# Performance work log

Measured on AMD Instinct MI355X. Metric: run time of the kernel, lower is better.

Reference implementation:

```python
import jax, jax.numpy as jnp
import numpy as np

NUM_HEADS = 4

def setup_inputs() -> dict:
    key = jax.random.key(0)
    ks = jax.random.split(key, 9)
    total_nodes, d, hidden, B = 262144, 256, 256, 8192
    node_embeddings = jax.random.normal(ks[0], (total_nodes, d), dtype=jnp.float32)
    segment_ids = jnp.sort(jax.random.randint(ks[1], (total_nodes,), 0, B, dtype=jnp.int32))
    # learnable params (MultiheadAttention packed qkv, out_proj, query, output_proj)
    s = 0.05
    query = jax.random.normal(ks[2], (1, d), dtype=jnp.float32)
    in_proj_w = jax.random.normal(ks[3], (3 * d, d), dtype=jnp.float32) * s
    in_proj_b = jax.random.normal(ks[4], (3 * d,), dtype=jnp.float32) * s
    out_proj_w = jax.random.normal(ks[5], (d, d), dtype=jnp.float32) * s
    out_proj_b = jax.random.normal(ks[6], (d,), dtype=jnp.float32) * s
    output_proj_w = jax.random.normal(ks[7], (hidden, d), dtype=jnp.float32) * s
    output_proj_b = jax.random.normal(ks[8], (hidden,), dtype=jnp.float32) * s
    return {
        "node_embeddings": node_embeddings,
        "query": query,
        "in_proj_w": in_proj_w,
        "in_proj_b": in_proj_b,
        "out_proj_w": out_proj_w,
        "out_proj_b": out_proj_b,
        "output_proj_w": output_proj_w,
        "output_proj_b": output_proj_b,
        "segment_ids": segment_ids,
        "batch_size": B,
    }


def reference(node_embeddings, query, in_proj_w, in_proj_b, out_proj_w, out_proj_b,
              output_proj_w, output_proj_b, segment_ids, batch_size):
    # Ragged single-query cross-attention pooling (eval mode: dropout off).
    N, d = node_embeddings.shape
    H = NUM_HEADS
    dh = d // H
    Wq, Wk, Wv = in_proj_w[:d], in_proj_w[d:2 * d], in_proj_w[2 * d:]
    bq, bk, bv = in_proj_b[:d], in_proj_b[d:2 * d], in_proj_b[2 * d:]
    # query is shared across all graphs; torch MHA scales q by 1/sqrt(dh)
    q = ((query @ Wq.T + bq) / jnp.sqrt(jnp.asarray(dh, node_embeddings.dtype))).reshape(H, dh)
    k = (node_embeddings @ Wk.T + bk).reshape(N, H, dh)
    v = (node_embeddings @ Wv.T + bv).reshape(N, H, dh)
    scores = jnp.einsum('nhd,hd->nh', k, q)  # [N, H]
    # segment-wise stable softmax over ragged node groups
    m = jax.ops.segment_max(scores, segment_ids, num_segments=batch_size)  # [B, H]
    m = jnp.where(jnp.isfinite(m), m, 0.0)
    e = jnp.exp(scores - m[segment_ids])  # [N, H]
    denom = jax.ops.segment_sum(e, segment_ids, num_segments=batch_size)  # [B, H]
    numer = jax.ops.segment_sum(e[:, :, None] * v, segment_ids, num_segments=batch_size)  # [B, H, dh]
    attn = jnp.where(denom[:, :, None] > 0, numer / jnp.maximum(denom[:, :, None], 1e-30), 0.0)
    pooled = attn.reshape(batch_size, d) @ out_proj_w.T + out_proj_b  # MHA out_proj
    out = pooled @ output_proj_w.T + output_proj_b  # [B, hidden]
    # empty graphs -> zeros (matches torch branch), not just bias
    counts = jax.ops.segment_sum(jnp.ones((N,), out.dtype), segment_ids, num_segments=batch_size)
    return jnp.where(counts[:, None] > 0, out, 0.0)
```

## Files before the change

kernel.cpp:

```cpp
#include <hip/hip_runtime.h>
#include <hip/hip_bf16.h>
#include <stdint.h>

typedef __attribute__((ext_vector_type(8))) short short8;
typedef __attribute__((ext_vector_type(4))) float f32x4;
typedef __attribute__((ext_vector_type(4))) float f32x4v;
typedef __attribute__((ext_vector_type(2))) float f32x2;

#define DEV static __device__ __forceinline__

DEV float half_red_bcast(float x) {
  int t;
  t = __builtin_amdgcn_update_dpp(0, __float_as_int(x), 0x111, 0xf, 0xf, true); x += __int_as_float(t);
  t = __builtin_amdgcn_update_dpp(0, __float_as_int(x), 0x112, 0xf, 0xf, true); x += __int_as_float(t);
  t = __builtin_amdgcn_update_dpp(0, __float_as_int(x), 0x114, 0xf, 0xf, true); x += __int_as_float(t);
  t = __builtin_amdgcn_update_dpp(0, __float_as_int(x), 0x118, 0xf, 0xf, true); x += __int_as_float(t);
  t = __builtin_amdgcn_update_dpp(0, __float_as_int(x), 0x142, 0xa, 0xf, true); x += __int_as_float(t);
  return __int_as_float(__builtin_amdgcn_ds_swizzle(__float_as_int(x), 0x3E0));
}

DEV void gload16(const void* g, void* lds) {
  __builtin_amdgcn_global_load_lds(
      (const __attribute__((address_space(1))) void*)g,
      (__attribute__((address_space(3))) void*)lds, 16, 0, 0);
}

#define LOG2E 1.44269504088896340736f

__global__ __launch_bounds__(256) void k_prep(
    const float* __restrict__ query, const float* __restrict__ in_w,
    const float* __restrict__ in_b, const int* __restrict__ seg,
    float* __restrict__ wq_ws, int* __restrict__ starts, int N, int B)
{
  __shared__ float sh[256];
  int t = threadIdx.x, bid = blockIdx.x;
  if (bid < 4) {
    float acc = in_b[t];
    for (int c = 0; c < 256; ++c) acc += query[c] * in_w[t * 256 + c];
    sh[t] = acc * 0.125f;
    __syncthreads();
    int h = bid;
    float a = 0.f;
    for (int j = 0; j < 64; ++j) a += sh[64 * h + j] * in_w[(256 + 64 * h + j) * 256 + t];
    wq_ws[h * 256 + t] = a * LOG2E;
  } else {
    int idx = (bid - 4) * 256 + t;
    if (idx < N) {
      int s = seg[idx];
      int prev = (idx == 0) ? -1 : seg[idx - 1];
      for (int x = prev + 1; x <= s; ++x) starts[x] = idx;
      if (idx == N - 1) for (int x = s + 1; x <= B; ++x) starts[x] = N;
    }
  }
}

__global__ __launch_bounds__(256, 4) void k_segattn(
    const float* __restrict__ emb, const int* __restrict__ starts,
    const float* __restrict__ wq_ws,
    float* __restrict__ mask, __hip_bfloat16* __restrict__ T, int B,
    const float* __restrict__ in_w, const float* __restrict__ in_b,
    const float* __restrict__ Wo, const float* __restrict__ bo,
    const float* __restrict__ Wu, const float* __restrict__ bu,
    __hip_bfloat16* __restrict__ mtt, float* __restrict__ btot)
{
  __shared__ float sh[256];
  int t = threadIdx.x;

  if (blockIdx.x < 257u) {
    int bid = blockIdx.x;
    if (bid < 256) {
      int u = bid;
      float wc = 0.f;
      for (int o = 0; o < 256; ++o) wc += Wu[u * 256 + o] * Wo[o * 256 + t];
      sh[t] = wc;
      __syncthreads();
      #pragma unroll
      for (int h = 0; h < 4; ++h) {
        float a = 0.f;
        for (int r = 0; r < 64; ++r) a += sh[64 * h + r] * in_w[(512 + 64 * h + r) * 256 + t];
        mtt[(size_t)u * 1024 + h * 256 + t] = __float2bfloat16(a);
      }
    } else {
      const float* bv = in_b + 512;
      float wob = 0.f;
      for (int c = 0; c < 256; ++c) wob += Wo[t * 256 + c] * bv[c];
      sh[t] = bo[t] + wob;
      __syncthreads();
      float a = bu[t];
      for (int o = 0; o < 256; ++o) a += Wu[t * 256 + o] * sh[o];
      btot[t] = a;
    }
    return;
  }

  int lane = t & 63;
  int g = lane >> 5, i = lane & 31, i8 = i * 8;
  int b = (blockIdx.x - 257) * 4 + (t >> 6);
  if (b >= B) return;
  int start = starts[b], end = starts[b + 1];
  __hip_bfloat16* Tb = T + (size_t)b * 1024;

  if (start >= end) {
    if (lane == 0) mask[b] = 0.f;
    if (lane < 32) {
      uint4 z = {0u, 0u, 0u, 0u};
      *(uint4*)(Tb + 0 * 256 + lane * 8) = z;
      *(uint4*)(Tb + 1 * 256 + lane * 8) = z;
      *(uint4*)(Tb + 2 * 256 + lane * 8) = z;
      *(uint4*)(Tb + 3 * 256 + lane * 8) = z;
    }
    return;
  }
  if (lane == 0) mask[b] = 1.f;

  f32x2 w[4][4];
  #pragma unroll
  for (int h = 0; h < 4; ++h) {
    const f32x2* wp = (const f32x2*)(wq_ws + h * 256 + i8);
    #pragma unroll
    for (int j = 0; j < 4; ++j) w[h][j] = wp[j];
  }

  float d[4] = {0.f, 0.f, 0.f, 0.f};
  f32x2 S[4][4] = {};

  int r0 = start + g;     if (r0 > end - 1) r0 = end - 1;
  int r1 = start + 2 + g; if (r1 > end - 1) r1 = end - 1;
  const float* p0 = emb + (size_t)r0 * 256 + i8;
  const float* p1 = emb + (size_t)r1 * 256 + i8;
  f32x4v c0 = *(const f32x4v*)p0, c1 = *(const f32x4v*)(p0 + 4);
  f32x4v n10 = *(const f32x4v*)p1, n11 = *(const f32x4v*)(p1 + 4);

  for (int p = start; p < end; p += 2) {
    int rn = p + 4 + g; if (rn > end - 1) rn = end - 1;
    const float* np = emb + (size_t)rn * 256 + i8;
    f32x4v L0 = *(const f32x4v*)np, L1 = *(const f32x4v*)(np + 4);

    f32x2 c0l = __builtin_shufflevector(c0, c0, 0, 1);
    f32x2 c0h = __builtin_shufflevector(c0, c0, 2, 3);
    f32x2 c1l = __builtin_shufflevector(c1, c1, 0, 1);
    f32x2 c1h = __builtin_shufflevector(c1, c1, 2, 3);

    f32x2 P0 = c0l * w[0][0] + c0h * w[0][1] + c1l * w[0][2] + c1h * w[0][3];
    f32x2 P1 = c0l * w[1][0] + c0h * w[1][1] + c1l * w[1][2] + c1h * w[1][3];
    f32x2 P2 = c0l * w[2][0] + c0h * w[2][1] + c1l * w[2][2] + c1h * w[2][3];
    f32x2 P3 = c0l * w[3][0] + c0h * w[3][1] + c1l * w[3][2] + c1h * w[3][3];

    float s0 = half_red_bcast(P0.x + P0.y);
    float s1 = half_red_bcast(P1.x + P1.y);
    float s2 = half_red_bcast(P2.x + P2.y);
    float s3 = half_red_bcast(P3.x + P3.y);

    if ((p + g) >= end) { s0 = -1e30f; s1 = -1e30f; s2 = -1e30f; s3 = -1e30f; }

    float e0 = __builtin_exp2f(s0); d[0] += e0;
    float e1 = __builtin_exp2f(s1); d[1] += e1;
    float e2 = __builtin_exp2f(s2); d[2] += e2;
    float e3 = __builtin_exp2f(s3); d[3] += e3;

#define ACC(h, e)                                                           \
    { f32x2 ev = {e, e};                                                    \
      S[h][0] += ev * c0l; S[h][1] += ev * c0h;                             \
      S[h][2] += ev * c1l; S[h][3] += ev * c1h; }
    ACC(0, e0) ACC(1, e1) ACC(2, e2) ACC(3, e3)
#undef ACC

    c0 = n10; c1 = n11; n10 = L0; n11 = L1;
  }

#define FIN(h)                                                              \
  { float od = __shfl_xor(d[h], 32);                                        \
    float sc = 1.f / (d[h] + od);                                           \
    float t0 = S[h][0].x * sc, t1 = S[h][0].y * sc;                         \
    float t2 = S[h][1].x * sc, t3 = S[h][1].y * sc;                         \
    float t4 = S[h][2].x * sc, t5 = S[h][2].y * sc;                         \
    float t6 = S[h][3].x * sc, t7 = S[h][3].y * sc;                         \
    t0 += __shfl_xor(t0, 32); t1 += __shfl_xor(t1, 32);                     \
    t2 += __shfl_xor(t2, 32); t3 += __shfl_xor(t3, 32);                     \
    t4 += __shfl_xor(t4, 32); t5 += __shfl_xor(t5, 32);                     \
    t6 += __shfl_xor(t6, 32); t7 += __shfl_xor(t7, 32);                     \
    if (g == 0) {                                                           \
      union { __hip_bfloat16 v[8]; uint4 u; } pk;                           \
      pk.v[0] = __float2bfloat16(t0); pk.v[1] = __float2bfloat16(t1);       \
      pk.v[2] = __float2bfloat16(t2); pk.v[3] = __float2bfloat16(t3);       \
      pk.v[4] = __float2bfloat16(t4); pk.v[5] = __float2bfloat16(t5);       \
      pk.v[6] = __float2bfloat16(t6); pk.v[7] = __float2bfloat16(t7);       \
      *(uint4*)(Tb + h * 256 + i8) = pk.u; } }
  FIN(0) FIN(1) FIN(2) FIN(3)
#undef FIN
}

__global__ __launch_bounds__(256) void k_out(
    const __hip_bfloat16* __restrict__ T, const __hip_bfloat16* __restrict__ mtt,
    const float* __restrict__ btot, const float* __restrict__ mask,
    float* __restrict__ out)
{
  __shared__ __align__(16) char smem[16384];
  char* As = smem;
  char* Bs = smem + 8192;
  int t = threadIdx.x;
  int l = t & 63, w = t >> 6;
  int wr = w >> 1, wc = w & 1;
  int tileM = blockIdx.x * 64, tileN = blockIdx.y * 64;

  const char* Tb = (const char*)T;
  const char* Mb = (const char*)mtt;
  int chunk = (l & 7) ^ ((l >> 3) & 7);
  f32x4 acc[2][2] = {};

  for (int kk = 0; kk < 1024; kk += 64) {
    #pragma unroll
    for (int i = 0; i < 2; ++i) {
      int row = (w * 2 + i) * 8 + (l >> 3);
      gload16(Tb + (size_t)(tileM + row) * 2048 + kk * 2 + chunk * 16,
              As + (w * 2 + i) * 1024);
      gload16(Mb + (size_t)(tileN + row) * 2048 + kk * 2 + chunk * 16,
              Bs + (w * 2 + i) * 1024);
    }
    __syncthreads();
    #pragma unroll
    for (int ks = 0; ks < 64; ks += 32) {
      short8 a[2], bf[2];
      int kbyte = (ks + (l >> 4) * 8) * 2;
      #pragma unroll
      for (int i = 0; i < 2; ++i) {
        int row = wr * 32 + i * 16 + (l & 15);
        a[i] = *(const short8*)(As + row * 128 + (kbyte ^ ((row & 7) << 4)));
        int crow = wc * 32 + i * 16 + (l & 15);
        bf[i] = *(const short8*)(Bs + crow * 128 + (kbyte ^ ((crow & 7) << 4)));
      }
      #pragma unroll
      for (int i = 0; i < 2; ++i)
        #pragma unroll
        for (int j = 0; j < 2; ++j)
          acc[i][j] = __builtin_amdgcn_mfma_f32_16x16x32_bf16(a[i], bf[j], acc[i][j], 0, 0, 0);
    }
    __syncthreads();
  }

  int cl = l & 15, rq = l >> 4;
  #pragma unroll
  for (int i = 0; i < 2; ++i)
    #pragma unroll
    for (int j = 0; j < 2; ++j) {
      int cg = tileN + wc * 32 + j * 16 + cl;
      float bt = btot[cg];
      #pragma unroll
      for (int r = 0; r < 4; ++r) {
        int rg = tileM + wr * 32 + i * 16 + rq * 4 + r;
        out[(size_t)rg * 256 + cg] = mask[rg] * (acc[i][j][r] + bt);
      }
    }
}

extern "C" void kernel_launch(void* const* d_in, const int* in_sizes, int n_in,
                              void* d_out, int out_size, void* d_ws, size_t ws_size,
                              hipStream_t stream) {
  const float* emb   = (const float*)d_in[0];
  const float* query = (const float*)d_in[1];
  const float* in_w  = (const float*)d_in[2];
  const float* in_b  = (const float*)d_in[3];
  const float* out_w = (const float*)d_in[4];
  const float* out_b = (const float*)d_in[5];
  const float* up_w  = (const float*)d_in[6];
  const float* up_b  = (const float*)d_in[7];
  const int*   seg   = (const int*)d_in[8];

  int N = in_sizes[0] / 256;
  int B = out_size / 256;

  char* wsb = (char*)d_ws;
  float* wq_ws  = (float*)(wsb + 0);
  float* btot   = (float*)(wsb + 8192);
  int*   starts = (int*)(wsb + 12288);
  float* maskp  = (float*)(wsb + 45312);
  __hip_bfloat16* mtt = (__hip_bfloat16*)(wsb + 78336);
  __hip_bfloat16* Tp  = (__hip_bfloat16*)(wsb + 602624);

  int nb_bounds = (N + 255) / 256;
  int nB = (B + 3) / 4;
  k_prep<<<dim3(4 + nb_bounds), dim3(256), 0, stream>>>(
      query, in_w, in_b, seg, wq_ws, starts, N, B);
  k_segattn<<<dim3(257 + nB), dim3(256), 0, stream>>>(
      emb, starts, wq_ws, maskp, Tp, B,
      in_w, in_b, out_w, out_b, up_w, up_b, mtt, btot);
  k_out<<<dim3(B / 64, 4), dim3(256), 0, stream>>>(Tp, mtt, btot, maskp, (float*)d_out);
}
```

Measured before the change: 83.98 us.

## Shrink segattn blocks to one wavefront per segment

Changes k_segattn from 256-thread blocks that each handle four segments to 64-thread blocks that each handle one segment, and launches B+260 blocks. The weight-folding prologue blocks are rewritten to loop over four column chunks per thread, and the bias computation is split across four blocks. The aim is to stop fast waves in a block from waiting on slow waves working on longer ragged segments, and to give the scheduler finer-grained work. In exchange there are many more small blocks, and the prologue blocks now do four times more serial work per thread.

```diff
diff --git a/kernel.cpp b/kernel.cpp
--- a/kernel.cpp
+++ b/kernel.cpp
@@ -54,7 +54,7 @@
   }
 }
 
-__global__ __launch_bounds__(256, 4) void k_segattn(
+__global__ __launch_bounds__(64, 4) void k_segattn(
     const float* __restrict__ emb, const int* __restrict__ starts,
     const float* __restrict__ wq_ws,
     float* __restrict__ mask, __hip_bfloat16* __restrict__ T, int B,
@@ -66,36 +66,50 @@
   __shared__ float sh[256];
   int t = threadIdx.x;
 
-  if (blockIdx.x < 257u) {
-    int bid = blockIdx.x;
-    if (bid < 256) {
-      int u = bid;
-      float wc = 0.f;
-      for (int o = 0; o < 256; ++o) wc += Wu[u * 256 + o] * Wo[o * 256 + t];
-      sh[t] = wc;
+  if (blockIdx.x < 260u) {
+    if (blockIdx.x < 256u) {
+      int u = blockIdx.x;
+      #pragma unroll
+      for (int j = 0; j < 4; ++j) {
+        int c = j * 64 + t;
+        float wc = 0.f;
+        for (int o = 0; o < 256; ++o) wc += Wu[u * 256 + o] * Wo[o * 256 + c];
+        sh[c] = wc;
+      }
       __syncthreads();
       #pragma unroll
       for (int h = 0; h < 4; ++h) {
-        float a = 0.f;
-        for (int r = 0; r < 64; ++r) a += sh[64 * h + r] * in_w[(512 + 64 * h + r) * 256 + t];
-        mtt[(size_t)u * 1024 + h * 256 + t] = __float2bfloat16(a);
+        #pragma unroll
+        for (int j = 0; j < 4; ++j) {
+          int c = j * 64 + t;
+          float a = 0.f;
+          for (int r = 0; r < 64; ++r)
+            a += sh[64 * h + r] * in_w[(512 + 64 * h + r) * 256 + c];
+          mtt[(size_t)u * 1024 + h * 256 + c] = __float2bfloat16(a);
+        }
       }
     } else {
+      int part = (blockIdx.x - 256) * 64;
       const float* bv = in_b + 512;
-      float wob = 0.f;
-      for (int c = 0; c < 256; ++c) wob += Wo[t * 256 + c] * bv[c];
-      sh[t] = bo[t] + wob;
+      #pragma unroll
+      for (int j = 0; j < 4; ++j) {
+        int c = j * 64 + t;
+        float wob = 0.f;
+        for (int o = 0; o < 256; ++o) wob += Wo[c * 256 + o] * bv[o];
+        sh[c] = bo[c] + wob;
+      }
       __syncthreads();
-      float a = bu[t];
-      for (int o = 0; o < 256; ++o) a += Wu[t * 256 + o] * sh[o];
-      btot[t] = a;
+      int c = part + t;
+      float a = bu[c];
+      for (int o = 0; o < 256; ++o) a += Wu[c * 256 + o] * sh[o];
+      btot[c] = a;
     }
     return;
   }
 
-  int lane = t & 63;
+  int lane = t;
   int g = lane >> 5, i = lane & 31, i8 = i * 8;
-  int b = (blockIdx.x - 257) * 4 + (t >> 6);
+  int b = blockIdx.x - 260;
   if (b >= B) return;
   int start = starts[b], end = starts[b + 1];
   __hip_bfloat16* Tb = T + (size_t)b * 1024;
@@ -278,10 +292,9 @@
   __hip_bfloat16* Tp  = (__hip_bfloat16*)(wsb + 602624);
 
   int nb_bounds = (N + 255) / 256;
-  int nB = (B + 3) / 4;
   k_prep<<<dim3(4 + nb_bounds), dim3(256), 0, stream>>>(
       query, in_w, in_b, seg, wq_ws, starts, N, B);
-  k_segattn<<<dim3(257 + nB), dim3(256), 0, stream>>>(
+  k_segattn<<<dim3(260 + B), dim3(64), 0, stream>>>(
       emb, starts, wq_ws, maskp, Tp, B,
       in_w, in_b, out_w, out_b, up_w, up_b, mtt, btot);
   k_out<<<dim3(B / 64, 4), dim3(256), 0, stream>>>(Tp, mtt, btot, maskp, (float*)d_out);
```

New measurement: 99.28 us. 1.18x slower.

## Split each segment across four waves and combine partial softmax sums in LDS

Applied to the files above, without the earlier changes.

Each block now handles one segment instead of four, and the segment's rows are split evenly across its four waves. Each wave builds partial numerators and denominators, writes them to shared memory, and after a barrier they are summed and normalized. This spreads the uneven segment lengths across more waves so the serial per-wave row loop is shorter. The cost is four times as many blocks, 16 KB of extra LDS per block, and a block barrier. Correctness still relies on the existing scheme, which omits the max-subtraction and accumulates unshifted exponentials in each wave.

```diff
diff --git a/kernel.cpp b/kernel.cpp
--- a/kernel.cpp
+++ b/kernel.cpp
@@ -63,10 +63,12 @@
     const float* __restrict__ Wu, const float* __restrict__ bu,
     __hip_bfloat16* __restrict__ mtt, float* __restrict__ btot)
 {
-  __shared__ float sh[256];
+  __shared__ float sm[16][256];
+  __shared__ float sd[16];
   int t = threadIdx.x;
 
   if (blockIdx.x < 257u) {
+    float* sh = sm[0];
     int bid = blockIdx.x;
     if (bid < 256) {
       int u = bid;
@@ -93,101 +95,108 @@
     return;
   }
 
+  int b = blockIdx.x - 257;
+  int start = starts[b], end = starts[b + 1];
+  __hip_bfloat16* Tb = T + (size_t)b * 1024;
+
+  if (start >= end) {
+    if (t == 0) mask[b] = 0.f;
+    if (t < 128) { uint4 z = {0u,0u,0u,0u}; *(uint4*)((char*)Tb + t * 16) = z; }
+    return;
+  }
+  if (t == 0) mask[b] = 1.f;
+
+  int w = t >> 6;
   int lane = t & 63;
   int g = lane >> 5, i = lane & 31, i8 = i * 8;
-  int b = (blockIdx.x - 257) * 4 + (t >> 6);
-  if (b >= B) return;
-  int start = starts[b], end = starts[b + 1];
-  __hip_bfloat16* Tb = T + (size_t)b * 1024;
-
-  if (start >= end) {
-    if (lane == 0) mask[b] = 0.f;
-    if (lane < 32) {
-      uint4 z = {0u, 0u, 0u, 0u};
-      *(uint4*)(Tb + 0 * 256 + lane * 8) = z;
-      *(uint4*)(Tb + 1 * 256 + lane * 8) = z;
-      *(uint4*)(Tb + 2 * 256 + lane * 8) = z;
-      *(uint4*)(Tb + 3 * 256 + lane * 8) = z;
-    }
-    return;
-  }
-  if (lane == 0) mask[b] = 1.f;
-
-  f32x2 w[4][4];
+
+  int len = end - start;
+  int per = (len + 3) >> 2;
+  int ws = start + w * per;
+  int we = ws + per; if (we > end) we = end;
+
+  f32x2 wq[4][4];
   #pragma unroll
   for (int h = 0; h < 4; ++h) {
     const f32x2* wp = (const f32x2*)(wq_ws + h * 256 + i8);
     #pragma unroll
-    for (int j = 0; j < 4; ++j) w[h][j] = wp[j];
+    for (int j = 0; j < 4; ++j) wq[h][j] = wp[j];
   }
 
   float d[4] = {0.f, 0.f, 0.f, 0.f};
   f32x2 S[4][4] = {};
 
-  int r0 = start + g;     if (r0 > end - 1) r0 = end - 1;
-  int r1 = start + 2 + g; if (r1 > end - 1) r1 = end - 1;
-  const float* p0 = emb + (size_t)r0 * 256 + i8;
-  const float* p1 = emb + (size_t)r1 * 256 + i8;
-  f32x4v c0 = *(const f32x4v*)p0, c1 = *(const f32x4v*)(p0 + 4);
-  f32x4v n10 = *(const f32x4v*)p1, n11 = *(const f32x4v*)(p1 + 4);
-
-  for (int p = start; p < end; p += 2) {
-    int rn = p + 4 + g; if (rn > end - 1) rn = end - 1;
-    const float* np = emb + (size_t)rn * 256 + i8;
-    f32x4v L0 = *(const f32x4v*)np, L1 = *(const f32x4v*)(np + 4);
-
-    f32x2 c0l = __builtin_shufflevector(c0, c0, 0, 1);
-    f32x2 c0h = __builtin_shufflevector(c0, c0, 2, 3);
-    f32x2 c1l = __builtin_shufflevector(c1, c1, 0, 1);
-    f32x2 c1h = __builtin_shufflevector(c1, c1, 2, 3);
-
-    f32x2 P0 = c0l * w[0][0] + c0h * w[0][1] + c1l * w[0][2] + c1h * w[0][3];
-    f32x2 P1 = c0l * w[1][0] + c0h * w[1][1] + c1l * w[1][2] + c1h * w[1][3];
-    f32x2 P2 = c0l * w[2][0] + c0h * w[2][1] + c1l * w[2][2] + c1h * w[2][3];
-    f32x2 P3 = c0l * w[3][0] + c0h * w[3][1] + c1l * w[3][2] + c1h * w[3][3];
-
-    float s0 = half_red_bcast(P0.x + P0.y);
-    float s1 = half_red_bcast(P1.x + P1.y);
-    float s2 = half_red_bcast(P2.x + P2.y);
-    float s3 = half_red_bcast(P3.x + P3.y);
-
-    if ((p + g) >= end) { s0 = -1e30f; s1 = -1e30f; s2 = -1e30f; s3 = -1e30f; }
-
-    float e0 = __builtin_exp2f(s0); d[0] += e0;
-    float e1 = __builtin_exp2f(s1); d[1] += e1;
-    float e2 = __builtin_exp2f(s2); d[2] += e2;
-    float e3 = __builtin_exp2f(s3); d[3] += e3;
+  if (ws < we) {
+    int r0 = ws + g;     if (r0 > we - 1) r0 = we - 1;
+    int r1 = ws + 2 + g; if (r1 > we - 1) r1 = we - 1;
+    const float* p0 = emb + (size_t)r0 * 256 + i8;
+    const float* p1 = emb + (size_t)r1 * 256 + i8;
+    f32x4v c0 = *(const f32x4v*)p0, c1 = *(const f32x4v*)(p0 + 4);
+    f32x4v n10 = *(const f32x4v*)p1, n11 = *(const f32x4v*)(p1 + 4);
+
+    for (int p = ws; p < we; p += 2) {
+      int rn = p + 4 + g; if (rn > we - 1) rn = we - 1;
+      const float* np = emb + (size_t)rn * 256 + i8;
+      f32x4v L0 = *(const f32x4v*)np, L1 = *(const f32x4v*)(np + 4);
+
+      f32x2 c0l = __builtin_shufflevector(c0, c0, 0, 1);
+      f32x2 c0h = __builtin_shufflevector(c0, c0, 2, 3);
+      f32x2 c1l = __builtin_shufflevector(c1, c1, 0, 1);
+      f32x2 c1h = __builtin_shufflevector(c1, c1, 2, 3);
+
+      f32x2 P0 = c0l * wq[0][0] + c0h * wq[0][1] + c1l * wq[0][2] + c1h * wq[0][3];
+      f32x2 P1 = c0l * wq[1][0] + c0h * wq[1][1] + c1l * wq[1][2] + c1h * wq[1][3];
+      f32x2 P2 = c0l * wq[2][0] + c0h * wq[2][1] + c1l * wq[2][2] + c1h * wq[2][3];
+      f32x2 P3 = c0l * wq[3][0] + c0h * wq[3][1] + c1l * wq[3][2] + c1h * wq[3][3];
+
+      float s0 = half_red_bcast(P0.x + P0.y);
+      float s1 = half_red_bcast(P1.x + P1.y);
+      float s2 = half_red_bcast(P2.x + P2.y);
+      float s3 = half_red_bcast(P3.x + P3.y);
+
+      if ((p + g) >= we) { s0 = -1e30f; s1 = -1e30f; s2 = -1e30f; s3 = -1e30f; }
+
+      float e0 = __builtin_exp2f(s0); d[0] += e0;
+      float e1 = __builtin_exp2f(s1); d[1] += e1;
+      float e2 = __builtin_exp2f(s2); d[2] += e2;
+      float e3 = __builtin_exp2f(s3); d[3] += e3;
 
 #define ACC(h, e)                                                           \
-    { f32x2 ev = {e, e};                                                    \
-      S[h][0] += ev * c0l; S[h][1] += ev * c0h;                             \
-      S[h][2] += ev * c1l; S[h][3] += ev * c1h; }
-    ACC(0, e0) ACC(1, e1) ACC(2, e2) ACC(3, e3)
+      { f32x2 ev = {e, e};                                                  \
+        S[h][0] += ev * c0l; S[h][1] += ev * c0h;                           \
+        S[h][2] += ev * c1l; S[h][3] += ev * c1h; }
+      ACC(0, e0) ACC(1, e1) ACC(2, e2) ACC(3, e3)
 #undef ACC
 
-    c0 = n10; c1 = n11; n10 = L0; n11 = L1;
-  }
-
-#define FIN(h)                                                              \
+      c0 = n10; c1 = n11; n10 = L0; n11 = L1;
+    }
+  }
+
+#define PUB(h)                                                              \
   { float od = __shfl_xor(d[h], 32);                                        \
-    float sc = 1.f / (d[h] + od);                                           \
-    float t0 = S[h][0].x * sc, t1 = S[h][0].y * sc;                         \
-    float t2 = S[h][1].x * sc, t3 = S[h][1].y * sc;                         \
-    float t4 = S[h][2].x * sc, t5 = S[h][2].y * sc;                         \
-    float t6 = S[h][3].x * sc, t7 = S[h][3].y * sc;                         \
+    float dt = d[h] + od;                                                   \
+    float t0 = S[h][0].x, t1 = S[h][0].y, t2 = S[h][1].x, t3 = S[h][1].y;   \
+    float t4 = S[h][2].x, t5 = S[h][2].y, t6 = S[h][3].x, t7 = S[h][3].y;   \
     t0 += __shfl_xor(t0, 32); t1 += __shfl_xor(t1, 32);                     \
     t2 += __shfl_xor(t2, 32); t3 += __shfl_xor(t3, 32);                     \
     t4 += __shfl_xor(t4, 32); t5 += __shfl_xor(t5, 32);                     \
     t6 += __shfl_xor(t6, 32); t7 += __shfl_xor(t7, 32);                     \
     if (g == 0) {                                                           \
-      union { __hip_bfloat16 v[8]; uint4 u; } pk;                           \
-      pk.v[0] = __float2bfloat16(t0); pk.v[1] = __float2bfloat16(t1);       \
-      pk.v[2] = __float2bfloat16(t2); pk.v[3] = __float2bfloat16(t3);       \
-      pk.v[4] = __float2bfloat16(t4); pk.v[5] = __float2bfloat16(t5);       \
-      pk.v[6] = __float2bfloat16(t6); pk.v[7] = __float2bfloat16(t7);       \
-      *(uint4*)(Tb + h * 256 + i8) = pk.u; } }
-  FIN(0) FIN(1) FIN(2) FIN(3)
-#undef FIN
+      float* row = sm[w * 4 + h];                                           \
+      f32x4v v0 = {t0, t1, t2, t3}, v1 = {t4, t5, t6, t7};                  \
+      *(f32x4v*)(row + i8) = v0; *(f32x4v*)(row + i8 + 4) = v1;             \
+      if (i == 0) sd[w * 4 + h] = dt; } }
+  PUB(0) PUB(1) PUB(2) PUB(3)
+#undef PUB
+
+  __syncthreads();
+
+  #pragma unroll
+  for (int h = 0; h < 4; ++h) {
+    float den = sd[h] + sd[4 + h] + sd[8 + h] + sd[12 + h];
+    float num = sm[h][t] + sm[4 + h][t] + sm[8 + h][t] + sm[12 + h][t];
+    Tb[h * 256 + t] = __float2bfloat16(num / den);
+  }
 }
 
 __global__ __launch_bounds__(256) void k_out(
@@ -278,10 +287,9 @@
   __hip_bfloat16* Tp  = (__hip_bfloat16*)(wsb + 602624);
 
   int nb_bounds = (N + 255) / 256;
-  int nB = (B + 3) / 4;
   k_prep<<<dim3(4 + nb_bounds), dim3(256), 0, stream>>>(
       query, in_w, in_b, seg, wq_ws, starts, N, B);
-  k_segattn<<<dim3(257 + nB), dim3(256), 0, stream>>>(
+  k_segattn<<<dim3(257 + B), dim3(256), 0, stream>>>(
       emb, starts, wq_ws, maskp, Tp, B,
       in_w, in_b, out_w, out_b, up_w, up_b, mtt, btot);
   k_out<<<dim3(B / 64, 4), dim3(256), 0, stream>>>(Tp, mtt, btot, maskp, (float*)d_out);
```

Measured after the change: 93.99 us. 1.12x slower.
